# Optimization experiments

Hardware: AMD Instinct MI355X
Metric: run time of the kernel (lower is better)

Reference implementation:

```python
import jax, jax.numpy as jnp
import numpy as np

N = 3072
SIGMA = 1.0
NORM_FACTOR = 90.4756
TWOPI = 2.0 * np.pi
NORM_CONST = NORM_FACTOR / TWOPI
A = 1.0 / (SIGMA * 2.0 ** 0.5)
SQRT_PI = np.pi ** 0.5


def setup_inputs() -> dict:
    key = jax.random.key(0)
    ks = jax.random.split(key, 6)
    q = jax.random.normal(ks[0], (N,), dtype=jnp.float32)
    r = jax.random.uniform(ks[1], (N, 3), dtype=jnp.float32) * 30.0  # 30A box
    cell = jnp.zeros((1, 3, 3), dtype=jnp.float32)  # det<1e-6 -> realspace path
    batch = jnp.zeros((N,), dtype=jnp.int32)
    u = jax.random.normal(ks[2], (N, 3), dtype=jnp.float32)
    kappa = jax.random.uniform(ks[3], (N,), dtype=jnp.float32)
    alpha = jax.random.uniform(ks[4], (N,), dtype=jnp.float32)
    return {"q": q, "r": r, "cell": cell, "batch": batch, "u": u, "kappa": kappa, "alpha": alpha}


def _ewald_realspace(q, r, u, kappa, alpha):
    # q:[n], r:[n,3], u:[n,3], kappa:[n], alpha:[n]; single batch, n_q=1 path
    n = q.shape[0]
    eye = jnp.eye(n, dtype=r.dtype)
    off = 1.0 - eye  # mask_off
    r_ij = r[None, :, :] - r[:, None, :]            # [n,n,3], r_j - r_i
    d2 = jnp.sum(r_ij * r_ij, axis=-1)
    rnorm = jnp.sqrt(d2 + eye)                      # diag padded with 1 for grad safety
    rinv = off / rnorm                              # 0 on diagonal
    rinv2 = rinv * rinv
    rinv3 = rinv2 * rinv
    erf = jax.scipy.special.erf(rnorm * A) * off    # 0 on diagonal
    gauss = jnp.exp(-(A * rnorm) ** 2) * off

    # charge-charge
    f_qq = erf * rinv * NORM_CONST
    e_phi = jnp.einsum('i,ij->j', q, f_qq)
    pot = 0.5 * jnp.dot(e_phi, q)

    # dipole kernels
    s1 = erf * rinv3 - (2.0 * A / SQRT_PI) * gauss * rinv2
    s2 = 3.0 * erf * rinv3 - (6.0 * A / SQRT_PI) * gauss * rinv2 - (4.0 * A ** 3 / SQRT_PI) * gauss

    # charge-dipole: f_qu[i,j,c] = s1[i,j]*r_ij[i,j,c]*NORM_CONST (contracted on the fly)
    ur = jnp.einsum('ic,ijc->ij', u, r_ij)          # u_i . r_ij
    e_phi_u = NORM_CONST * jnp.einsum('ij,ij->j', s1, ur)
    e_phi = e_phi + e_phi_u
    pot = pot + jnp.dot(e_phi_u, q)

    # dipole-dipole: f_uu = NORM_CONST*(s2 * rhat rhat^T - s1 * I), contracted without [n,n,3,3]
    rhat = r_ij * rinv[..., None]
    ai = jnp.einsum('ic,ijc->ij', u, rhat)          # u_i . rhat_ij
    bj = jnp.einsum('jc,ijc->ij', u, rhat)          # u_j . rhat_ij
    uu = u @ u.T
    pot = pot - 0.5 * NORM_CONST * (jnp.sum(s2 * ai * bj) - jnp.sum(s1 * uu))

    # induced charges (remove_self_interaction=True: no self terms)
    q_induced = -kappa * e_phi
    pot = pot + 0.5 * jnp.dot(e_phi, q_induced)

    # electric field (alpha is not None -> computed)
    e_field = NORM_CONST * jnp.einsum('i,ij,ijc->jc', q, s1, r_ij)
    E_u = NORM_CONST * (jnp.einsum('ij,ijd->jd', s2 * ai, rhat) - s1.T @ u)
    e_field = e_field + E_u

    # induced dipoles (alpha scalar per node)
    u_induced = e_field * alpha[:, None]
    pot = pot - 0.5 * jnp.sum(e_field * u_induced)

    return pot.reshape(1), q_induced, u_induced


def reference(q, r, cell, batch, u, kappa, alpha):
    # cell is zeros (det < 1e-6) and batch is all-zeros -> single-system realspace branch
    return _ewald_realspace(q, r, u, kappa, alpha)
```

## Files before the change

### kernel.cpp

```cpp
#include <hip/hip_runtime.h>
#include <hip/hip_bf16.h>

#define NATOMS 3072
#define CHUNKS 32
#define WPB 4
#define IPB (NATOMS / CHUNKS)
#define IPW (IPB / WPB)

static_assert(IPB * CHUNKS == NATOMS, "i-partition must cover all atoms");
static_assert(IPW * WPB == IPB, "wave split must cover block chunk");

constexpr float NCf = (float)(90.4756 / (2.0 * 3.14159265358979323846));
constexpr float Af = 0.70710678118654752f;
constexpr float Cf = 0.79788456080286536f;

__global__ __launch_bounds__(256)
void ewald_main(const float* __restrict__ q, const float* __restrict__ r,
                const float* __restrict__ u, float* __restrict__ part,
                float* __restrict__ out) {
  const int lane = threadIdx.x & 63;
  const int w = threadIdx.x >> 6;
  const int j = blockIdx.x * 64 + lane;

  if (blockIdx.x == 0 && blockIdx.y == 0 && threadIdx.x == 0) out[0] = 0.0f;

  __shared__ float4 sPU[2 * IPB];
  const int i0 = blockIdx.y * IPB;
  for (int t = threadIdx.x; t < IPB; t += 256) {
    const int i = i0 + t;
    sPU[2 * t + 0] = make_float4(r[3 * i + 0], r[3 * i + 1], r[3 * i + 2], q[i]);
    sPU[2 * t + 1] = make_float4(u[3 * i + 0], u[3 * i + 1], u[3 * i + 2], 0.0f);
  }
  const float pjx = r[3 * j + 0];
  const float pjy = r[3 * j + 1];
  const float pjz = r[3 * j + 2];
  __syncthreads();

  float acc0 = 0.f, acc1 = 0.f, acc2 = 0.f, acc3 = 0.f;
  float acc4 = 0.f, acc5 = 0.f, acc6 = 0.f, acc7 = 0.f;

  const int jt = j - i0;
  const int t0 = w * IPW;
#pragma unroll 2
  for (int t = t0; t < t0 + IPW; ++t) {
    const float4 pi = sPU[2 * t + 0];
    const float4 ui = sPU[2 * t + 1];
    const float dx = pjx - pi.x;
    const float dy = pjy - pi.y;
    const float dz = pjz - pi.z;
    float d2 = fmaf(dx, dx, fmaf(dy, dy, dz * dz));
    if (t == jt) d2 = 1e18f;

    const float rinv = __builtin_amdgcn_rsqf(d2);
    const float rinv2 = rinv * rinv;
    const float rinv3 = rinv2 * rinv;
    const float ur = ui.x * dx + ui.y * dy + ui.z * dz;

    float e0, s1, s2;
    if (__any(d2 < 18.0f)) {
      const float rnorm = d2 * rinv;
      const float g0 = __expf(-0.5f * d2);
      const float tt =
          __builtin_amdgcn_rcpf(fmaf(0.3275911f * Af, rnorm, 1.0f));
      const float poly =
          tt * (0.254829592f +
                tt * (-0.284496736f +
                      tt * (1.421413741f +
                            tt * (-1.453152027f + tt * 1.061405429f))));
      const float erfv = fmaf(-poly, g0, 1.0f);
      const float cg = Cf * g0;
      e0 = erfv * rinv;
      s1 = erfv * rinv3 - cg * rinv2;
      s2 = fmaf(3.0f, s1, -cg);
    } else {
      e0 = rinv;
      s1 = rinv3;
      s2 = 3.0f * rinv3;
    }

    acc0 = fmaf(pi.w, e0, acc0);
    acc1 = fmaf(s1, ur, acc1);
    const float qs1 = pi.w * s1;
    acc2 = fmaf(qs1, dx, acc2);
    acc3 = fmaf(qs1, dy, acc3);
    acc4 = fmaf(qs1, dz, acc4);
    const float t2 = s2 * ur * rinv2;
    acc5 = fmaf(t2, dx, fmaf(-s1, ui.x, acc5));
    acc6 = fmaf(t2, dy, fmaf(-s1, ui.y, acc6));
    acc7 = fmaf(t2, dz, fmaf(-s1, ui.z, acc7));
  }

  __shared__ float red[(WPB - 1) * 64 * 8];
  __syncthreads();
  if (w > 0) {
    float* dst = &red[((w - 1) * 64 + lane) * 8];
    dst[0] = acc0; dst[1] = acc1; dst[2] = acc2; dst[3] = acc3;
    dst[4] = acc4; dst[5] = acc5; dst[6] = acc6; dst[7] = acc7;
  }
  __syncthreads();
  if (w == 0) {
#pragma unroll
    for (int ww = 0; ww < WPB - 1; ++ww) {
      const float* src = &red[(ww * 64 + lane) * 8];
      acc0 += src[0]; acc1 += src[1]; acc2 += src[2]; acc3 += src[3];
      acc4 += src[4]; acc5 += src[5]; acc6 += src[6]; acc7 += src[7];
    }
    float4* dst = (float4*)&part[((size_t)blockIdx.y * NATOMS + j) * 8];
    dst[0] = make_float4(acc0, acc1, acc2, acc3);
    dst[1] = make_float4(acc4, acc5, acc6, acc7);
  }
}

__global__ __launch_bounds__(256)
void ewald_finalize(const float* __restrict__ part, const float* __restrict__ q,
                    const float* __restrict__ u, const float* __restrict__ kappa,
                    const float* __restrict__ alpha, float* __restrict__ out) {
  const int j = blockIdx.x * blockDim.x + threadIdx.x;

  float s[8] = {0.f, 0.f, 0.f, 0.f, 0.f, 0.f, 0.f, 0.f};
#pragma unroll
  for (int c = 0; c < CHUNKS; ++c) {
    const float4* src = (const float4*)&part[((size_t)c * NATOMS + j) * 8];
    const float4 a = src[0];
    const float4 b = src[1];
    s[0] += a.x; s[1] += a.y; s[2] += a.z; s[3] += a.w;
    s[4] += b.x; s[5] += b.y; s[6] += b.z; s[7] += b.w;
  }

  const float e_phi = NCf * (s[0] + s[1]);
  const float Eux = NCf * s[5];
  const float Euy = NCf * s[6];
  const float Euz = NCf * s[7];
  const float efx = NCf * s[2] + Eux;
  const float efy = NCf * s[3] + Euy;
  const float efz = NCf * s[4] + Euz;

  const float qj = q[j];
  const float kj = kappa[j];
  const float aj = alpha[j];
  const float ujx = u[3 * j + 0];
  const float ujy = u[3 * j + 1];
  const float ujz = u[3 * j + 2];

  out[1 + j] = -kj * e_phi;
  out[1 + NATOMS + 3 * j + 0] = aj * efx;
  out[1 + NATOMS + 3 * j + 1] = aj * efy;
  out[1 + NATOMS + 3 * j + 2] = aj * efz;

  float potj = 0.5f * NCf * s[0] * qj
             + NCf * s[1] * qj
             - 0.5f * (ujx * Eux + ujy * Euy + ujz * Euz)
             - 0.5f * kj * e_phi * e_phi
             - 0.5f * aj * (efx * efx + efy * efy + efz * efz);

#pragma unroll
  for (int m = 32; m >= 1; m >>= 1) potj += __shfl_xor(potj, m, 64);
  __shared__ float lred[4];
  const int lane = threadIdx.x & 63;
  const int wid = threadIdx.x >> 6;
  if (lane == 0) lred[wid] = potj;
  __syncthreads();
  if (threadIdx.x == 0) {
    atomicAdd(out, lred[0] + lred[1] + lred[2] + lred[3]);
  }
}

extern "C" void kernel_launch(void* const* d_in, const int* in_sizes, int n_in,
                              void* d_out, int out_size, void* d_ws,
                              size_t ws_size, hipStream_t stream) {
  const float* q = (const float*)d_in[0];
  const float* r = (const float*)d_in[1];
  const float* u = (const float*)d_in[4];
  const float* kappa = (const float*)d_in[5];
  const float* alpha = (const float*)d_in[6];
  float* out = (float*)d_out;

  float* part = (float*)d_ws;

  ewald_main<<<dim3(NATOMS / 64, CHUNKS), 256, 0, stream>>>(q, r, u, part, out);
  ewald_finalize<<<dim3(NATOMS / 256), 256, 0, stream>>>(part, q, u, kappa,
                                                         alpha, out);
}
```

Baseline: 83.96 us.

## Pre-pack atom data into global float4 buffer and specialize diagonal-free wave loops

Adds a pack kernel that writes r, q and u into interleaved float4 records in workspace. The main kernel now reads those records directly from global memory with wave-uniform addresses instead of staging them in LDS, which removes the first __syncthreads. It also templates the pair loop so waves whose i-range cannot contain j skip the diagonal check, raises the unroll factor to 6, and fuses a few multiply-adds. The cost is an extra kernel launch and scalar or broadcast global loads in place of LDS reads.

```diff
diff --git a/kernel.cpp b/kernel.cpp
--- a/kernel.cpp
+++ b/kernel.cpp
@@ -1,5 +1,4 @@
 #include <hip/hip_runtime.h>
-#include <hip/hip_bf16.h>
 
 #define NATOMS 3072
 #define CHUNKS 32
@@ -15,46 +14,39 @@
 constexpr float Cf = 0.79788456080286536f;
 
 __global__ __launch_bounds__(256)
-void ewald_main(const float* __restrict__ q, const float* __restrict__ r,
-                const float* __restrict__ u, float* __restrict__ part,
+void ewald_pack(const float* __restrict__ q, const float* __restrict__ r,
+                const float* __restrict__ u, float4* __restrict__ pu,
                 float* __restrict__ out) {
-  const int lane = threadIdx.x & 63;
-  const int w = threadIdx.x >> 6;
-  const int j = blockIdx.x * 64 + lane;
-
-  if (blockIdx.x == 0 && blockIdx.y == 0 && threadIdx.x == 0) out[0] = 0.0f;
-
-  __shared__ float4 sPU[2 * IPB];
-  const int i0 = blockIdx.y * IPB;
-  for (int t = threadIdx.x; t < IPB; t += 256) {
-    const int i = i0 + t;
-    sPU[2 * t + 0] = make_float4(r[3 * i + 0], r[3 * i + 1], r[3 * i + 2], q[i]);
-    sPU[2 * t + 1] = make_float4(u[3 * i + 0], u[3 * i + 1], u[3 * i + 2], 0.0f);
-  }
-  const float pjx = r[3 * j + 0];
-  const float pjy = r[3 * j + 1];
-  const float pjz = r[3 * j + 2];
-  __syncthreads();
-
-  float acc0 = 0.f, acc1 = 0.f, acc2 = 0.f, acc3 = 0.f;
-  float acc4 = 0.f, acc5 = 0.f, acc6 = 0.f, acc7 = 0.f;
-
-  const int jt = j - i0;
-  const int t0 = w * IPW;
-#pragma unroll 2
+  const int i = blockIdx.x * 256 + threadIdx.x;
+  if (i == 0) out[0] = 0.0f;
+  if (i < NATOMS) {
+    pu[2 * i + 0] = make_float4(r[3 * i + 0], r[3 * i + 1], r[3 * i + 2], q[i]);
+    pu[2 * i + 1] = make_float4(u[3 * i + 0], u[3 * i + 1], u[3 * i + 2], 0.0f);
+  }
+}
+
+template <bool DIAG>
+__device__ __forceinline__ void pair_loop(
+    const float4* __restrict__ pu, int i0, int t0, int jt,
+    float pjx, float pjy, float pjz,
+    float& acc0, float& acc1, float& acc2, float& acc3,
+    float& acc4, float& acc5, float& acc6, float& acc7) {
+#pragma unroll 6
   for (int t = t0; t < t0 + IPW; ++t) {
-    const float4 pi = sPU[2 * t + 0];
-    const float4 ui = sPU[2 * t + 1];
+    const float4 pi = pu[2 * (i0 + t) + 0];
+    const float4 ui = pu[2 * (i0 + t) + 1];
     const float dx = pjx - pi.x;
     const float dy = pjy - pi.y;
     const float dz = pjz - pi.z;
     float d2 = fmaf(dx, dx, fmaf(dy, dy, dz * dz));
-    if (t == jt) d2 = 1e18f;
+    if (DIAG) {
+      if (t == jt) d2 = 1e18f;
+    }
 
     const float rinv = __builtin_amdgcn_rsqf(d2);
     const float rinv2 = rinv * rinv;
     const float rinv3 = rinv2 * rinv;
-    const float ur = ui.x * dx + ui.y * dy + ui.z * dz;
+    const float ur = fmaf(ui.x, dx, fmaf(ui.y, dy, ui.z * dz));
 
     float e0, s1, s2;
     if (__any(d2 < 18.0f)) {
@@ -70,7 +62,7 @@
       const float erfv = fmaf(-poly, g0, 1.0f);
       const float cg = Cf * g0;
       e0 = erfv * rinv;
-      s1 = erfv * rinv3 - cg * rinv2;
+      s1 = fmaf(erfv, rinv3, -(cg * rinv2));
       s2 = fmaf(3.0f, s1, -cg);
     } else {
       e0 = rinv;
@@ -89,9 +81,34 @@
     acc6 = fmaf(t2, dy, fmaf(-s1, ui.y, acc6));
     acc7 = fmaf(t2, dz, fmaf(-s1, ui.z, acc7));
   }
+}
+
+__global__ __launch_bounds__(256)
+void ewald_main(const float4* __restrict__ pu, float* __restrict__ part) {
+  const int lane = threadIdx.x & 63;
+  const int w = threadIdx.x >> 6;
+  const int j = blockIdx.x * 64 + lane;
+  const int i0 = blockIdx.y * IPB;
+
+  const float4 pj = pu[2 * j + 0];
+  const float pjx = pj.x, pjy = pj.y, pjz = pj.z;
+
+  float acc0 = 0.f, acc1 = 0.f, acc2 = 0.f, acc3 = 0.f;
+  float acc4 = 0.f, acc5 = 0.f, acc6 = 0.f, acc7 = 0.f;
+
+  const int jt = j - i0;
+  const int t0 = w * IPW;
+
+  const int jlo = blockIdx.x * 64;
+  const bool diagW = (jlo < i0 + t0 + IPW) && (i0 + t0 < jlo + 64);
+  if (diagW)
+    pair_loop<true>(pu, i0, t0, jt, pjx, pjy, pjz,
+                    acc0, acc1, acc2, acc3, acc4, acc5, acc6, acc7);
+  else
+    pair_loop<false>(pu, i0, t0, jt, pjx, pjy, pjz,
+                     acc0, acc1, acc2, acc3, acc4, acc5, acc6, acc7);
 
   __shared__ float red[(WPB - 1) * 64 * 8];
-  __syncthreads();
   if (w > 0) {
     float* dst = &red[((w - 1) * 64 + lane) * 8];
     dst[0] = acc0; dst[1] = acc1; dst[2] = acc2; dst[3] = acc3;
@@ -176,8 +193,11 @@
   float* out = (float*)d_out;
 
   float* part = (float*)d_ws;
-
-  ewald_main<<<dim3(NATOMS / 64, CHUNKS), 256, 0, stream>>>(q, r, u, part, out);
+  float4* pu = (float4*)((char*)d_ws +
+                         (size_t)CHUNKS * NATOMS * 8 * sizeof(float));
+
+  ewald_pack<<<dim3(NATOMS / 256), 256, 0, stream>>>(q, r, u, pu, out);
+  ewald_main<<<dim3(NATOMS / 64, CHUNKS), 256, 0, stream>>>(pu, part);
   ewald_finalize<<<dim3(NATOMS / 256), 256, 0, stream>>>(part, q, u, kappa,
                                                          alpha, out);
 }
```

New measurement: 91.31 us. 8.7% more time.
